# Optimization experiments

Hardware: AMD Instinct MI355X
Metric: run time of the kernel (lower is better)

Reference implementation:

```python
import jax, jax.numpy as jnp
import numpy as np

T, B, D, H, F, O = 256, 512, 256, 512, 64, 1


def setup_inputs() -> dict:
    key = jax.random.key(0)
    ks = jax.random.split(key, 16)
    s = 0.05
    return {
        "inputs": jax.random.normal(ks[0], (T, B, D), jnp.float32),
        "hidden_init": jnp.zeros((B, H), jnp.float32),
        "cell_init": jnp.zeros((B, H), jnp.float32),
        # LSTMCell params (torch gate order: i, f, g, o)
        "W_ih": jax.random.normal(ks[1], (4 * H, D), jnp.float32) * s,
        "W_hh": jax.random.normal(ks[2], (4 * H, H), jnp.float32) * s,
        "b_ih": jax.random.normal(ks[3], (4 * H,), jnp.float32) * s,
        "b_hh": jax.random.normal(ks[4], (4 * H,), jnp.float32) * s,
        # Attention fc: hidden_dim -> 1
        "attn_w": jax.random.normal(ks[5], (1, H), jnp.float32) * s,
        "attn_b": jax.random.normal(ks[6], (1,), jnp.float32) * s,
        # Output MLP: H->F, F->F, F->F//2, F//2->O
        "W1": jax.random.normal(ks[7], (F, H), jnp.float32) * s,
        "b1": jax.random.normal(ks[8], (F,), jnp.float32) * s,
        "W2": jax.random.normal(ks[9], (F, F), jnp.float32) * s,
        "b2": jax.random.normal(ks[10], (F,), jnp.float32) * s,
        "W3": jax.random.normal(ks[11], (F // 2, F), jnp.float32) * s,
        "b3": jax.random.normal(ks[12], (F // 2,), jnp.float32) * s,
        "W4": jax.random.normal(ks[13], (O, F // 2), jnp.float32) * s,
        "b4": jax.random.normal(ks[14], (O,), jnp.float32) * s,
    }


def _lstm_scan(inputs, h0, c0, W_ih, W_hh, b_ih, b_hh):
    def step(carry, x):
        h, c = carry
        gates = x @ W_ih.T + b_ih + h @ W_hh.T + b_hh  # (B, 4H)
        i, f, g, o = jnp.split(gates, 4, axis=-1)
        c = jax.nn.sigmoid(f) * c + jax.nn.sigmoid(i) * jnp.tanh(g)
        h = jax.nn.sigmoid(o) * jnp.tanh(c)
        return (h, c), h

    (hT, cT), hs = jax.lax.scan(step, (h0, c0), inputs)
    return hT, cT, hs  # hs: (T, B, H)


def reference(inputs, hidden_init, cell_init, W_ih, W_hh, b_ih, b_hh,
              attn_w, attn_b, W1, b1, W2, b2, W3, b3, W4, b4):
    hT, cT, hs = _lstm_scan(inputs, hidden_init, cell_init, W_ih, W_hh, b_ih, b_hh)
    hs = jnp.transpose(hs, (1, 0, 2))            # (B, T, H) == torch.stack(hiddens, dim=1)
    scores = hs @ attn_w.T + attn_b              # (B, T, 1)
    weights = jax.nn.softmax(scores, axis=1)     # softmax over time
    context = jnp.sum(weights * hs, axis=1)      # (B, H)
    x = jnp.tanh(context @ W1.T + b1)
    x = jnp.tanh(x @ W2.T + b2)
    x = jnp.tanh(x @ W3.T + b3)
    out = x @ W4.T + b4                          # (B, O)
    return out, hT, cT
```

## Files before the change

kernel.cpp:

```cpp
#include <hip/hip_runtime.h>


typedef _Float16 f16x8 __attribute__((ext_vector_type(8)));
typedef short    s16x8 __attribute__((ext_vector_type(8)));
typedef float    f32x4 __attribute__((ext_vector_type(4)));

union F16U { f16x8 v; _Float16 e[8]; };

__device__ __forceinline__ float h2f(unsigned short b) {
    return (float)__builtin_bit_cast(_Float16, b);
}
__device__ __forceinline__ unsigned short f2h(float f) {
    return __builtin_bit_cast(unsigned short, (_Float16)f);
}
__device__ __forceinline__ float sigf(float x) { return 1.0f / (1.0f + __expf(-x)); }
__device__ __forceinline__ float tanh_(float x) {
    float e = __expf(-2.0f * fabsf(x));
    float r = (1.0f - e) / (1.0f + e);
    return x < 0.0f ? -r : r;
}
__device__ __forceinline__ unsigned umin_(unsigned a, unsigned b) { return a < b ? a : b; }

__device__ __forceinline__ f16x8 loadA32(const float* p) {
    float4 a = *(const float4*)p, b = *(const float4*)(p + 4);
    F16U r;
    r.e[0]=(_Float16)a.x; r.e[1]=(_Float16)a.y; r.e[2]=(_Float16)a.z; r.e[3]=(_Float16)a.w;
    r.e[4]=(_Float16)b.x; r.e[5]=(_Float16)b.y; r.e[6]=(_Float16)b.z; r.e[7]=(_Float16)b.w;
    return r.v;
}

#define MFMA16(a, b, c) __builtin_amdgcn_mfma_f32_16x16x32_f16((a), (b), (c), 0, 0, 0)
#define BIDX(g, kc) (((g) * 16 + lj) * 96 + ((((kc) * 4) + lq) ^ vg[(g)]))

__device__ __forceinline__ void issue_x(const float* x_t, int arow, int lq, float4* xpf) {
    const float* xb = x_t + (size_t)arow * 256 + lq * 8;
#pragma unroll
    for (int i = 0; i < 8; ++i) {
        asm volatile("global_load_dwordx4 %0, %1, off offset:%c2"
                     : "=v"(xpf[2 * i]) : "v"(xb), "i"(i * 128));
        asm volatile("global_load_dwordx4 %0, %1, off offset:%c2"
                     : "=v"(xpf[2 * i + 1]) : "v"(xb), "i"(i * 128 + 16));
    }
}

__device__ __forceinline__ void gemm_x_reg(const float4* xpf, const f16x8* Wl,
    int lj, int lq, const int* vg,
    f32x4& acc0, f32x4& acc1, f32x4& acc2, f32x4& acc3)
{
    asm volatile("s_waitcnt vmcnt(0)" ::: "memory");
    __builtin_amdgcn_sched_barrier(0);
#pragma unroll
    for (int kc = 0; kc < 8; ++kc) {
        float4 a = xpf[2 * kc], b = xpf[2 * kc + 1];
        F16U r;
        r.e[0]=(_Float16)a.x; r.e[1]=(_Float16)a.y; r.e[2]=(_Float16)a.z; r.e[3]=(_Float16)a.w;
        r.e[4]=(_Float16)b.x; r.e[5]=(_Float16)b.y; r.e[6]=(_Float16)b.z; r.e[7]=(_Float16)b.w;
        acc0 = MFMA16(r.v, Wl[BIDX(0, kc)], acc0);
        acc1 = MFMA16(r.v, Wl[BIDX(1, kc)], acc1);
        acc2 = MFMA16(r.v, Wl[BIDX(2, kc)], acc2);
        acc3 = MFMA16(r.v, Wl[BIDX(3, kc)], acc3);
    }
}

__device__ __forceinline__ void wait_flags(const uint4* fbase, int l, unsigned target) {
    if (l < 32) {
        const uint4* p = fbase + l;
        unsigned m;
        do {
            uint4 v;
            asm volatile("global_load_dwordx4 %0, %1, off sc0 sc1" : "=v"(v) : "v"(p));
            asm volatile("s_waitcnt vmcnt(0)" ::: "memory");
            m = umin_(umin_(v.x, v.y), umin_(v.z, v.w));
        } while (m < target);
    }
    __builtin_amdgcn_sched_barrier(0);
}

template<bool SC>
__device__ __forceinline__ void gemm_h(const unsigned short* hsrc, const f16x8* Wl,
    int arow, int lj, int lq, const int* vg,
    const unsigned short* ap_dot, const unsigned short* ap_ctx,
    uint4& hdot, uint2& hctx,
    f32x4& acc0, f32x4& acc1, f32x4& acc2, f32x4& acc3)
{
    const unsigned short* hp = hsrc + (size_t)arow * 512 + lq * 8;
    s16x8 hf[16];
#pragma unroll
    for (int i = 0; i < 16; ++i) {
        if constexpr (SC)
            asm volatile("global_load_dwordx4 %0, %1, off offset:%c2 sc0 sc1"
                         : "=v"(hf[i]) : "v"(hp), "i"(i * 64));
        else
            asm volatile("global_load_dwordx4 %0, %1, off offset:%c2"
                         : "=v"(hf[i]) : "v"(hp), "i"(i * 64));
    }
    if constexpr (SC) {
        asm volatile("global_load_dwordx4 %0, %1, off sc0 sc1" : "=v"(hdot) : "v"(ap_dot));
        asm volatile("global_load_dwordx2 %0, %1, off sc0 sc1" : "=v"(hctx) : "v"(ap_ctx));
    } else {
        asm volatile("global_load_dwordx4 %0, %1, off" : "=v"(hdot) : "v"(ap_dot));
        asm volatile("global_load_dwordx2 %0, %1, off" : "=v"(hctx) : "v"(ap_ctx));
    }

    asm volatile("s_waitcnt vmcnt(10)" ::: "memory");
    __builtin_amdgcn_sched_barrier(0);
#pragma unroll
    for (int kc = 8; kc < 16; ++kc) {
        f16x8 a = __builtin_bit_cast(f16x8, hf[kc - 8]);
        acc0 = MFMA16(a, Wl[BIDX(0, kc)], acc0);
        acc1 = MFMA16(a, Wl[BIDX(1, kc)], acc1);
        acc2 = MFMA16(a, Wl[BIDX(2, kc)], acc2);
        acc3 = MFMA16(a, Wl[BIDX(3, kc)], acc3);
    }
    asm volatile("s_waitcnt vmcnt(2)" ::: "memory");
    __builtin_amdgcn_sched_barrier(0);
#pragma unroll
    for (int kc = 16; kc < 24; ++kc) {
        f16x8 a = __builtin_bit_cast(f16x8, hf[kc - 8]);
        acc0 = MFMA16(a, Wl[BIDX(0, kc)], acc0);
        acc1 = MFMA16(a, Wl[BIDX(1, kc)], acc1);
        acc2 = MFMA16(a, Wl[BIDX(2, kc)], acc2);
        acc3 = MFMA16(a, Wl[BIDX(3, kc)], acc3);
    }
}

__device__ __forceinline__ void gemm_h_init(const float* hsrc, const f16x8* Wl,
    int arow, int lj, int lq, const int* vg,
    f32x4& acc0, f32x4& acc1, f32x4& acc2, f32x4& acc3)
{
    const float* hb = hsrc + (size_t)arow * 512 + lq * 8;
#pragma unroll
    for (int kc = 8; kc < 24; ++kc) {
        f16x8 a = loadA32(hb + (kc - 8) * 32);
        acc0 = MFMA16(a, Wl[BIDX(0, kc)], acc0);
        acc1 = MFMA16(a, Wl[BIDX(1, kc)], acc1);
        acc2 = MFMA16(a, Wl[BIDX(2, kc)], acc2);
        acc3 = MFMA16(a, Wl[BIDX(3, kc)], acc3);
    }
}

__device__ __forceinline__ void attn_apply(uint4 hd, uint2 hc, const float* wv8,
    float s_bias, float& m_r, float& l_r, float ctx[4])
{
    float p = h2f((unsigned short)(hd.x & 0xffffu)) * wv8[0]
            + h2f((unsigned short)(hd.x >> 16))     * wv8[1]
            + h2f((unsigned short)(hd.y & 0xffffu)) * wv8[2]
            + h2f((unsigned short)(hd.y >> 16))     * wv8[3]
            + h2f((unsigned short)(hd.z & 0xffffu)) * wv8[4]
            + h2f((unsigned short)(hd.z >> 16))     * wv8[5]
            + h2f((unsigned short)(hd.w & 0xffffu)) * wv8[6]
            + h2f((unsigned short)(hd.w >> 16))     * wv8[7];
#pragma unroll
    for (int off = 32; off > 0; off >>= 1) p += __shfl_xor(p, off);
    float s = p + s_bias;
    float m_new = fmaxf(m_r, s);
    float scale = __expf(m_r - m_new);
    float pr    = __expf(s - m_new);
    ctx[0] = ctx[0] * scale + pr * h2f((unsigned short)(hc.x & 0xffffu));
    ctx[1] = ctx[1] * scale + pr * h2f((unsigned short)(hc.x >> 16));
    ctx[2] = ctx[2] * scale + pr * h2f((unsigned short)(hc.y & 0xffffu));
    ctx[3] = ctx[3] * scale + pr * h2f((unsigned short)(hc.y >> 16));
    l_r = l_r * scale + pr;
    m_r = m_new;
}

#define SMEM_BYTES 104192

template<bool HIST>
__device__ __forceinline__ void lstm_body(
    const float* __restrict__ xg,
    const float* __restrict__ hinit, const float* __restrict__ cinit,
    const float* __restrict__ W_ih, const float* __restrict__ W_hh,
    const float* __restrict__ b_ih, const float* __restrict__ b_hh,
    const float* __restrict__ attn_w, const float* __restrict__ attn_b,
    const float* __restrict__ W1, const float* __restrict__ b1,
    const float* __restrict__ W2, const float* __restrict__ b2,
    const float* __restrict__ W3, const float* __restrict__ b3,
    const float* __restrict__ W4, const float* __restrict__ b4,
    float* __restrict__ out,
    unsigned short* __restrict__ hbA, unsigned short* __restrict__ hbB,
    unsigned* __restrict__ flags)
{
    extern __shared__ char smem[];
    f16x8* Wl    = (f16x8*)smem;
    float* bsum  = (float*)(smem + 98304);
    float* xmlp  = (float*)(smem + 98304 + 512);
    float* x1s   = xmlp + 1024;
    float* x2s   = x1s + 128;
    float* x3s   = x2s + 128;

    const int tid = threadIdx.x, bid = blockIdx.x;
    const int mt = bid & 7, nt = bid >> 3;
    const int hc0 = nt * 16;
    const int w = tid >> 6, l = tid & 63;
    const int lj = l & 15, lq = l >> 4;

    int vg[4];
#pragma unroll
    for (int g = 0; g < 4; ++g) {
        int q = g * 16 + lj;
        vg[g] = ((q >> 3) ^ q) & 7;
    }

    {
        int q = tid >> 2, si = tid & 3;
        int vq = ((q >> 3) ^ q) & 7;
        int grow = (q >> 4) * 512 + hc0 + (q & 15);
        const float* ih = W_ih + (size_t)grow * 256;
        const float* hh = W_hh + (size_t)grow * 512;
        for (int cc = 0; cc < 24; ++cc) {
            int s = si * 24 + cc;
            int k0 = s * 8;
            const float* p = (k0 < 256) ? (ih + k0) : (hh + (k0 - 256));
            float4 a = *(const float4*)p, b = *(const float4*)(p + 4);
            F16U r;
            r.e[0]=(_Float16)a.x; r.e[1]=(_Float16)a.y; r.e[2]=(_Float16)a.z; r.e[3]=(_Float16)a.w;
            r.e[4]=(_Float16)b.x; r.e[5]=(_Float16)b.y; r.e[6]=(_Float16)b.z; r.e[7]=(_Float16)b.w;
            Wl[q * 96 + (s ^ vq)] = r.v;
        }
        if (tid < 64) {
            int gr = (tid >> 4) * 512 + hc0 + (tid & 15);
            bsum[tid] = b_ih[gr] + b_hh[gr];
        }
    }
    __syncthreads();

    const int arow = mt * 64 + w * 16 + lj;
    const int crow = mt * 64 + w * 16 + lq * 4;
    const int ccol = hc0 + lj;
    float creg[4];
#pragma unroll
    for (int r = 0; r < 4; ++r)
        creg[r] = cinit[(size_t)(crow + r) * 512 + ccol];

    float m_r = -__builtin_inff(), l_r = 0.f;
    float ctx[4] = {0.f, 0.f, 0.f, 0.f};
    uint4 hdot = {0, 0, 0, 0}; uint2 hctx = {0, 0};
    const int attr0 = mt * 64 + nt * 2;
    const int arow_at = attr0 + (w >> 1);
    const float s_bias = attn_b[0];
    float wv8[8];
    {
        float4 a = *(const float4*)(attn_w + l * 8);
        float4 b = *(const float4*)(attn_w + l * 8 + 4);
        wv8[0]=a.x; wv8[1]=a.y; wv8[2]=a.z; wv8[3]=a.w;
        wv8[4]=b.x; wv8[5]=b.y; wv8[6]=b.z; wv8[7]=b.w;
    }
    float bs0 = bsum[lj], bs1 = bsum[16 + lj], bs2 = bsum[32 + lj], bs3 = bsum[48 + lj];

    const size_t aoff_dot = (size_t)arow_at * 512 + l * 8;
    const size_t aoff_ctx = (size_t)arow_at * 512 + (w & 1) * 256 + l * 4;
    const uint4* fbase = (const uint4*)flags + mt * 32;
    unsigned* myflag = flags + (size_t)(mt * 32 + nt) * 4 + w;

    float4 xpf[16];
    issue_x(xg, arow, lq, xpf);

    for (int t = 0; t < 256; ++t) {
        unsigned short* hb_cur;
        const unsigned short* hb_prev;
        if constexpr (HIST) {
            hb_cur  = hbA + (size_t)t * 262144;
            hb_prev = hb_cur - 262144;
        } else {
            hb_cur  = (t & 1) ? hbB : hbA;
            hb_prev = (t & 1) ? hbA : hbB;
        }

        f32x4 acc0 = {0,0,0,0}, acc1 = {0,0,0,0}, acc2 = {0,0,0,0}, acc3 = {0,0,0,0};
        gemm_x_reg(xpf, Wl, lj, lq, vg, acc0, acc1, acc2, acc3);

        if (t >= 2) attn_apply(hdot, hctx, wv8, s_bias, m_r, l_r, ctx);

        if (t > 0) {
            wait_flags(fbase, l, (unsigned)t);
            gemm_h<!HIST>(hb_prev, Wl, arow, lj, lq, vg,
                          hb_prev + aoff_dot, hb_prev + aoff_ctx, hdot, hctx,
                          acc0, acc1, acc2, acc3);
        } else {
            gemm_h_init(hinit, Wl, arow, lj, lq, vg, acc0, acc1, acc2, acc3);
        }

#pragma unroll
        for (int r = 0; r < 4; ++r) {
            float ii = sigf(acc0[r] + bs0);
            float ff = sigf(acc1[r] + bs1);
            float gt = tanh_(acc2[r] + bs2);
            float oo = sigf(acc3[r] + bs3);
            float cn = ff * creg[r] + ii * gt;
            creg[r] = cn;
            float hv = oo * tanh_(cn);
            size_t off = (size_t)(crow + r) * 512 + ccol;
            unsigned short hvs = f2h(hv);
            unsigned short* sp = hb_cur + off;
            asm volatile("global_store_short %0, %1, off sc0 sc1"
                         :: "v"(sp), "v"(hvs) : "memory");
            if (t == 255) out[512 + off] = hv;
        }

        const float* xnext = xg + (size_t)(t < 255 ? t + 1 : 255) * 131072;
        issue_x(xnext, arow, lq, xpf);

        asm volatile("s_waitcnt vmcnt(16)" ::: "memory");
        if (l == 0) {
            unsigned fv = (unsigned)(t + 1);
            asm volatile("global_store_dword %0, %1, off sc0 sc1"
                         :: "v"(myflag), "v"(fv) : "memory");
        }
    }

    attn_apply(hdot, hctx, wv8, s_bias, m_r, l_r, ctx);
    wait_flags(fbase, l, 256u);
    {
        const unsigned short* hlast = HIST ? (hbA + (size_t)255 * 262144) : hbB;
        const unsigned short* hp = hlast + aoff_dot;
        const unsigned short* hc = hlast + aoff_ctx;
        if constexpr (HIST) {
            asm volatile("global_load_dwordx4 %0, %1, off" : "=v"(hdot) : "v"(hp));
            asm volatile("global_load_dwordx2 %0, %1, off" : "=v"(hctx) : "v"(hc));
        } else {
            asm volatile("global_load_dwordx4 %0, %1, off sc0 sc1" : "=v"(hdot) : "v"(hp));
            asm volatile("global_load_dwordx2 %0, %1, off sc0 sc1" : "=v"(hctx) : "v"(hc));
        }
        asm volatile("s_waitcnt vmcnt(0)" ::: "memory");
        __builtin_amdgcn_sched_barrier(0);
        attn_apply(hdot, hctx, wv8, s_bias, m_r, l_r, ctx);
    }

#pragma unroll
    for (int r = 0; r < 4; ++r)
        out[512 + 262144 + (size_t)(crow + r) * 512 + ccol] = creg[r];

    {
        float linv = 1.0f / l_r;
        int row = tid >> 7, coff = (tid & 127) * 4;
#pragma unroll
        for (int i = 0; i < 4; ++i) xmlp[row * 512 + coff + i] = ctx[i] * linv;
    }
    __syncthreads();
    if (tid < 128) {
        int r = tid >> 6, f = tid & 63;
        const float* wp = W1 + (size_t)f * 512;
        const float* xp = xmlp + r * 512;
        float a = b1[f];
        for (int j = 0; j < 512; ++j) a = fmaf(xp[j], wp[j], a);
        x1s[r * 64 + f] = tanh_(a);
    }
    __syncthreads();
    if (tid < 128) {
        int r = tid >> 6, f = tid & 63;
        const float* wp = W2 + f * 64;
        const float* xp = x1s + r * 64;
        float a = b2[f];
        for (int j = 0; j < 64; ++j) a = fmaf(xp[j], wp[j], a);
        x2s[r * 64 + f] = tanh_(a);
    }
    __syncthreads();
    if (tid < 64) {
        int r = tid >> 5, f = tid & 31;
        const float* wp = W3 + f * 64;
        const float* xp = x2s + r * 64;
        float a = b3[f];
        for (int j = 0; j < 64; ++j) a = fmaf(xp[j], wp[j], a);
        x3s[r * 32 + f] = tanh_(a);
    }
    __syncthreads();
    if (tid < 2) {
        const float* xp = x3s + tid * 32;
        float a = b4[0];
        for (int j = 0; j < 32; ++j) a = fmaf(xp[j], W4[j], a);
        out[attr0 + tid] = a;
    }
}

__global__ __launch_bounds__(256, 1) void lstm_hist(
    const float* __restrict__ xg,
    const float* __restrict__ hinit, const float* __restrict__ cinit,
    const float* __restrict__ W_ih, const float* __restrict__ W_hh,
    const float* __restrict__ b_ih, const float* __restrict__ b_hh,
    const float* __restrict__ attn_w, const float* __restrict__ attn_b,
    const float* __restrict__ W1, const float* __restrict__ b1,
    const float* __restrict__ W2, const float* __restrict__ b2,
    const float* __restrict__ W3, const float* __restrict__ b3,
    const float* __restrict__ W4, const float* __restrict__ b4,
    float* __restrict__ out,
    unsigned short* __restrict__ hs, unsigned* __restrict__ flags)
{
    lstm_body<true>(xg, hinit, cinit, W_ih, W_hh, b_ih, b_hh, attn_w, attn_b,
                    W1, b1, W2, b2, W3, b3, W4, b4, out, hs, nullptr, flags);
}

__global__ __launch_bounds__(256, 1) void lstm_legacy(
    const float* __restrict__ xg,
    const float* __restrict__ hinit, const float* __restrict__ cinit,
    const float* __restrict__ W_ih, const float* __restrict__ W_hh,
    const float* __restrict__ b_ih, const float* __restrict__ b_hh,
    const float* __restrict__ attn_w, const float* __restrict__ attn_b,
    const float* __restrict__ W1, const float* __restrict__ b1,
    const float* __restrict__ W2, const float* __restrict__ b2,
    const float* __restrict__ W3, const float* __restrict__ b3,
    const float* __restrict__ W4, const float* __restrict__ b4,
    float* __restrict__ out,
    unsigned short* __restrict__ hb0, unsigned short* __restrict__ hb1,
    unsigned* __restrict__ flags)
{
    lstm_body<false>(xg, hinit, cinit, W_ih, W_hh, b_ih, b_hh, attn_w, attn_b,
                     W1, b1, W2, b2, W3, b3, W4, b4, out, hb0, hb1, flags);
}

extern "C" void kernel_launch(void* const* d_in, const int* in_sizes, int n_in,
                              void* d_out, int out_size, void* d_ws, size_t ws_size,
                              hipStream_t stream) {
    const float* xg     = (const float*)d_in[0];
    const float* hinit  = (const float*)d_in[1];
    const float* cinit  = (const float*)d_in[2];
    const float* W_ih   = (const float*)d_in[3];
    const float* W_hh   = (const float*)d_in[4];
    const float* b_ih   = (const float*)d_in[5];
    const float* b_hh   = (const float*)d_in[6];
    const float* attn_w = (const float*)d_in[7];
    const float* attn_b = (const float*)d_in[8];
    const float* W1 = (const float*)d_in[9],  *b1 = (const float*)d_in[10];
    const float* W2 = (const float*)d_in[11], *b2 = (const float*)d_in[12];
    const float* W3 = (const float*)d_in[13], *b3 = (const float*)d_in[14];
    const float* W4 = (const float*)d_in[15], *b4 = (const float*)d_in[16];

    const size_t HS_BYTES = (size_t)256 * 512 * 512 * 2;
    if (ws_size >= HS_BYTES + 4096) {
        unsigned short* hs = (unsigned short*)d_ws;
        unsigned* flags = (unsigned*)((char*)d_ws + HS_BYTES);
        hipMemsetAsync(flags, 0, 4096, stream);
        hipFuncSetAttribute((const void*)lstm_hist,
                            hipFuncAttributeMaxDynamicSharedMemorySize, SMEM_BYTES);
        lstm_hist<<<256, 256, SMEM_BYTES, stream>>>(
            xg, hinit, cinit, W_ih, W_hh, b_ih, b_hh, attn_w, attn_b,
            W1, b1, W2, b2, W3, b3, W4, b4,
            (float*)d_out, hs, flags);
    } else {
        unsigned short* hb0 = (unsigned short*)d_ws;
        unsigned short* hb1 = hb0 + 262144;
        unsigned* flags = (unsigned*)((char*)d_ws + 1048576);
        hipMemsetAsync(flags, 0, 4096, stream);
        hipFuncSetAttribute((const void*)lstm_legacy,
                            hipFuncAttributeMaxDynamicSharedMemorySize, SMEM_BYTES);
        lstm_legacy<<<256, 256, SMEM_BYTES, stream>>>(
            xg, hinit, cinit, W_ih, W_hh, b_ih, b_hh, attn_w, attn_b,
            W1, b1, W2, b2, W3, b3, W4, b4,
            (float*)d_out, hb0, hb1, flags);
    }
}
```

Before: 1.668 ms.

## Pre-convert inputs to fp16 in a separate pass and prefetch flag poll

Adds a separate grid-stride kernel that converts the whole fp32 input sequence to fp16 in workspace before the persistent LSTM kernel runs. The recurrent kernel then prefetches half as many bytes per timestep and feeds them straight into MFMA with no per-step conversion. It also issues the first cross-block flag poll early, overlapping it with the input GEMM. This costs an extra full pass over the input and more workspace, and the fallback path now needs the workspace to hold the fp16 copy too.

```diff
diff --git a/kernel.cpp b/kernel.cpp
--- a/kernel.cpp
+++ b/kernel.cpp
@@ -32,34 +32,26 @@
 #define MFMA16(a, b, c) __builtin_amdgcn_mfma_f32_16x16x32_f16((a), (b), (c), 0, 0, 0)
 #define BIDX(g, kc) (((g) * 16 + lj) * 96 + ((((kc) * 4) + lq) ^ vg[(g)]))
 
-__device__ __forceinline__ void issue_x(const float* x_t, int arow, int lq, float4* xpf) {
-    const float* xb = x_t + (size_t)arow * 256 + lq * 8;
-#pragma unroll
-    for (int i = 0; i < 8; ++i) {
+__device__ __forceinline__ void issue_xh(const unsigned short* xh_t, int arow, int lq, s16x8* xpf) {
+    const unsigned short* xb = xh_t + (size_t)arow * 256 + lq * 8;
+#pragma unroll
+    for (int i = 0; i < 8; ++i)
         asm volatile("global_load_dwordx4 %0, %1, off offset:%c2"
-                     : "=v"(xpf[2 * i]) : "v"(xb), "i"(i * 128));
-        asm volatile("global_load_dwordx4 %0, %1, off offset:%c2"
-                     : "=v"(xpf[2 * i + 1]) : "v"(xb), "i"(i * 128 + 16));
-    }
-}
-
-__device__ __forceinline__ void gemm_x_reg(const float4* xpf, const f16x8* Wl,
-    int lj, int lq, const int* vg,
-    f32x4& acc0, f32x4& acc1, f32x4& acc2, f32x4& acc3)
-{
-    asm volatile("s_waitcnt vmcnt(0)" ::: "memory");
+                     : "=v"(xpf[i]) : "v"(xb), "i"(i * 64));
+}
+
+__device__ __forceinline__ void wait_flags_pre(uint4 pre, const uint4* fbase, int l, unsigned target) {
+    if (l < 32) {
+        unsigned m = umin_(umin_(pre.x, pre.y), umin_(pre.z, pre.w));
+        const uint4* p = fbase + l;
+        while (m < target) {
+            uint4 v;
+            asm volatile("global_load_dwordx4 %0, %1, off sc0 sc1" : "=v"(v) : "v"(p));
+            asm volatile("s_waitcnt vmcnt(0)" ::: "memory");
+            m = umin_(umin_(v.x, v.y), umin_(v.z, v.w));
+        }
+    }
     __builtin_amdgcn_sched_barrier(0);
-#pragma unroll
-    for (int kc = 0; kc < 8; ++kc) {
-        float4 a = xpf[2 * kc], b = xpf[2 * kc + 1];
-        F16U r;
-        r.e[0]=(_Float16)a.x; r.e[1]=(_Float16)a.y; r.e[2]=(_Float16)a.z; r.e[3]=(_Float16)a.w;
-        r.e[4]=(_Float16)b.x; r.e[5]=(_Float16)b.y; r.e[6]=(_Float16)b.z; r.e[7]=(_Float16)b.w;
-        acc0 = MFMA16(r.v, Wl[BIDX(0, kc)], acc0);
-        acc1 = MFMA16(r.v, Wl[BIDX(1, kc)], acc1);
-        acc2 = MFMA16(r.v, Wl[BIDX(2, kc)], acc2);
-        acc3 = MFMA16(r.v, Wl[BIDX(3, kc)], acc3);
-    }
 }
 
 __device__ __forceinline__ void wait_flags(const uint4* fbase, int l, unsigned target) {
@@ -166,9 +158,24 @@
 
 #define SMEM_BYTES 104192
 
+__global__ __launch_bounds__(256) void xcvt(const float* __restrict__ xg,
+                                            unsigned short* __restrict__ xh)
+{
+    const size_t N = 33554432ull;
+    size_t stride = (size_t)gridDim.x * 256 * 8;
+    for (size_t i = ((size_t)blockIdx.x * 256 + threadIdx.x) * 8; i < N; i += stride) {
+        float4 a = *(const float4*)(xg + i);
+        float4 b = *(const float4*)(xg + i + 4);
+        F16U r;
+        r.e[0]=(_Float16)a.x; r.e[1]=(_Float16)a.y; r.e[2]=(_Float16)a.z; r.e[3]=(_Float16)a.w;
+        r.e[4]=(_Float16)b.x; r.e[5]=(_Float16)b.y; r.e[6]=(_Float16)b.z; r.e[7]=(_Float16)b.w;
+        *(f16x8*)(xh + i) = r.v;
+    }
+}
+
 template<bool HIST>
 __device__ __forceinline__ void lstm_body(
-    const float* __restrict__ xg,
+    const unsigned short* __restrict__ xh,
     const float* __restrict__ hinit, const float* __restrict__ cinit,
     const float* __restrict__ W_ih, const float* __restrict__ W_hh,
     const float* __restrict__ b_ih, const float* __restrict__ b_hh,
@@ -212,11 +219,7 @@
             int s = si * 24 + cc;
             int k0 = s * 8;
             const float* p = (k0 < 256) ? (ih + k0) : (hh + (k0 - 256));
-            float4 a = *(const float4*)p, b = *(const float4*)(p + 4);
-            F16U r;
-            r.e[0]=(_Float16)a.x; r.e[1]=(_Float16)a.y; r.e[2]=(_Float16)a.z; r.e[3]=(_Float16)a.w;
-            r.e[4]=(_Float16)b.x; r.e[5]=(_Float16)b.y; r.e[6]=(_Float16)b.z; r.e[7]=(_Float16)b.w;
-            Wl[q * 96 + (s ^ vq)] = r.v;
+            Wl[q * 96 + (s ^ vq)] = loadA32(p);
         }
         if (tid < 64) {
             int gr = (tid >> 4) * 512 + hc0 + (tid & 15);
@@ -252,9 +255,10 @@
     const size_t aoff_ctx = (size_t)arow_at * 512 + (w & 1) * 256 + l * 4;
     const uint4* fbase = (const uint4*)flags + mt * 32;
     unsigned* myflag = flags + (size_t)(mt * 32 + nt) * 4 + w;
-
-    float4 xpf[16];
-    issue_x(xg, arow, lq, xpf);
+    const uint4* mypoll = fbase + (l < 32 ? l : 0);
+
+    s16x8 xpf[8];
+    issue_xh(xh, arow, lq, xpf);
 
     for (int t = 0; t < 256; ++t) {
         unsigned short* hb_cur;
@@ -267,13 +271,28 @@
             hb_prev = (t & 1) ? hbA : hbB;
         }
 
+        asm volatile("s_waitcnt vmcnt(0)" ::: "memory");
+        __builtin_amdgcn_sched_barrier(0);
+        uint4 pre = {0, 0, 0, 0};
+        if (l < 32)
+            asm volatile("global_load_dwordx4 %0, %1, off sc0 sc1" : "=v"(pre) : "v"(mypoll));
+
         f32x4 acc0 = {0,0,0,0}, acc1 = {0,0,0,0}, acc2 = {0,0,0,0}, acc3 = {0,0,0,0};
-        gemm_x_reg(xpf, Wl, lj, lq, vg, acc0, acc1, acc2, acc3);
+#pragma unroll
+        for (int kc = 0; kc < 8; ++kc) {
+            f16x8 a = __builtin_bit_cast(f16x8, xpf[kc]);
+            acc0 = MFMA16(a, Wl[BIDX(0, kc)], acc0);
+            acc1 = MFMA16(a, Wl[BIDX(1, kc)], acc1);
+            acc2 = MFMA16(a, Wl[BIDX(2, kc)], acc2);
+            acc3 = MFMA16(a, Wl[BIDX(3, kc)], acc3);
+        }
 
         if (t >= 2) attn_apply(hdot, hctx, wv8, s_bias, m_r, l_r, ctx);
 
         if (t > 0) {
-            wait_flags(fbase, l, (unsigned)t);
+            asm volatile("s_waitcnt vmcnt(0)" ::: "memory");
+            __builtin_amdgcn_sched_barrier(0);
+            wait_flags_pre(pre, fbase, l, (unsigned)t);
             gemm_h<!HIST>(hb_prev, Wl, arow, lj, lq, vg,
                           hb_prev + aoff_dot, hb_prev + aoff_ctx, hdot, hctx,
                           acc0, acc1, acc2, acc3);
@@ -298,10 +317,10 @@
             if (t == 255) out[512 + off] = hv;
         }
 
-        const float* xnext = xg + (size_t)(t < 255 ? t + 1 : 255) * 131072;
-        issue_x(xnext, arow, lq, xpf);
-
-        asm volatile("s_waitcnt vmcnt(16)" ::: "memory");
+        const unsigned short* xnext = xh + (size_t)(t < 255 ? t + 1 : 255) * 131072;
+        issue_xh(xnext, arow, lq, xpf);
+
+        asm volatile("s_waitcnt vmcnt(8)" ::: "memory");
         if (l == 0) {
             unsigned fv = (unsigned)(t + 1);
             asm volatile("global_store_dword %0, %1, off sc0 sc1"
@@ -374,7 +393,7 @@
 }
 
 __global__ __launch_bounds__(256, 1) void lstm_hist(
-    const float* __restrict__ xg,
+    const unsigned short* __restrict__ xh,
     const float* __restrict__ hinit, const float* __restrict__ cinit,
     const float* __restrict__ W_ih, const float* __restrict__ W_hh,
     const float* __restrict__ b_ih, const float* __restrict__ b_hh,
@@ -386,12 +405,12 @@
     float* __restrict__ out,
     unsigned short* __restrict__ hs, unsigned* __restrict__ flags)
 {
-    lstm_body<true>(xg, hinit, cinit, W_ih, W_hh, b_ih, b_hh, attn_w, attn_b,
+    lstm_body<true>(xh, hinit, cinit, W_ih, W_hh, b_ih, b_hh, attn_w, attn_b,
                     W1, b1, W2, b2, W3, b3, W4, b4, out, hs, nullptr, flags);
 }
 
-__global__ __launch_bounds__(256, 1) void lstm_legacy(
-    const float* __restrict__ xg,
+__global__ __launch_bounds__(256, 1) void lstm_pp(
+    const unsigned short* __restrict__ xh,
     const float* __restrict__ hinit, const float* __restrict__ cinit,
     const float* __restrict__ W_ih, const float* __restrict__ W_hh,
     const float* __restrict__ b_ih, const float* __restrict__ b_hh,
@@ -404,7 +423,7 @@
     unsigned short* __restrict__ hb0, unsigned short* __restrict__ hb1,
     unsigned* __restrict__ flags)
 {
-    lstm_body<false>(xg, hinit, cinit, W_ih, W_hh, b_ih, b_hh, attn_w, attn_b,
+    lstm_body<false>(xh, hinit, cinit, W_ih, W_hh, b_ih, b_hh, attn_w, attn_b,
                      W1, b1, W2, b2, W3, b3, W4, b4, out, hb0, hb1, flags);
 }
 
@@ -425,26 +444,33 @@
     const float* W3 = (const float*)d_in[13], *b3 = (const float*)d_in[14];
     const float* W4 = (const float*)d_in[15], *b4 = (const float*)d_in[16];
 
-    const size_t HS_BYTES = (size_t)256 * 512 * 512 * 2;
-    if (ws_size >= HS_BYTES + 4096) {
-        unsigned short* hs = (unsigned short*)d_ws;
-        unsigned* flags = (unsigned*)((char*)d_ws + HS_BYTES);
+    const size_t XH_BYTES = 67108864ull;
+    const size_t HS_BYTES = 134217728ull;
+    const size_t PP_BYTES = 1048576ull;
+
+    unsigned short* xh = (unsigned short*)d_ws;
+    hipFuncSetAttribute((const void*)lstm_hist,
+                        hipFuncAttributeMaxDynamicSharedMemorySize, SMEM_BYTES);
+    hipFuncSetAttribute((const void*)lstm_pp,
+                        hipFuncAttributeMaxDynamicSharedMemorySize, SMEM_BYTES);
+
+    xcvt<<<2048, 256, 0, stream>>>(xg, xh);
+
+    if (ws_size >= XH_BYTES + HS_BYTES + 4096) {
+        unsigned short* hs = (unsigned short*)((char*)d_ws + XH_BYTES);
+        unsigned* flags = (unsigned*)((char*)d_ws + XH_BYTES + HS_BYTES);
         hipMemsetAsync(flags, 0, 4096, stream);
-        hipFuncSetAttribute((const void*)lstm_hist,
-                            hipFuncAttributeMaxDynamicSharedMemorySize, SMEM_BYTES);
         lstm_hist<<<256, 256, SMEM_BYTES, stream>>>(
-            xg, hinit, cinit, W_ih, W_hh, b_ih, b_hh, attn_w, attn_b,
+            xh, hinit, cinit, W_ih, W_hh, b_ih, b_hh, attn_w, attn_b,
             W1, b1, W2, b2, W3, b3, W4, b4,
             (float*)d_out, hs, flags);
     } else {
-        unsigned short* hb0 = (unsigned short*)d_ws;
+        unsigned short* hb0 = (unsigned short*)((char*)d_ws + XH_BYTES);
         unsigned short* hb1 = hb0 + 262144;
-        unsigned* flags = (unsigned*)((char*)d_ws + 1048576);
+        unsigned* flags = (unsigned*)((char*)d_ws + XH_BYTES + PP_BYTES);
         hipMemsetAsync(flags, 0, 4096, stream);
-        hipFuncSetAttribute((const void*)lstm_legacy,
-                            hipFuncAttributeMaxDynamicSharedMemorySize, SMEM_BYTES);
-        lstm_legacy<<<256, 256, SMEM_BYTES, stream>>>(
-            xg, hinit, cinit, W_ih, W_hh, b_ih, b_hh, attn_w, attn_b,
+        lstm_pp<<<256, 256, SMEM_BYTES, stream>>>(
+            xh, hinit, cinit, W_ih, W_hh, b_ih, b_hh, attn_w, attn_b,
             W1, b1, W2, b2, W3, b3, W4, b4,
             (float*)d_out, hb0, hb1, flags);
     }
```

After: 2.980 ms. +78.6%, slower.
